# Optimization experiments

Hardware: AMD Instinct MI355X
Metric: run time of the kernel (lower is better)

Reference implementation:

```python
import jax, jax.numpy as jnp
import numpy as np

PAD_IDX = 0
PROTON_MASS = 1.007276
WATER_MASS = 18.010565
CO_MASS = 27.994915
MASS_TOL = 0.5
TEMPERATURE = 0.1
HUBER_DELTA = 0.2
CE_WEIGHT = 1.0
SPEC_WEIGHT = 0.1
T, B, S, V = 6, 512, 40, 28
N_PEAKS = 512


def setup_inputs() -> dict:
    key = jax.random.key(0)
    ks = jax.random.split(key, 7)
    all_logits = jax.random.normal(ks[0], (T, B, S, V), dtype=jnp.float32)
    targets = jax.random.randint(ks[1], (B, S), 0, V, dtype=jnp.int32)
    target_mask = jax.random.uniform(ks[2], (B, S)) > 0.2
    # observed peak m/z values in a realistic 100..2000 Da window, sorted per spectrum
    observed_masses = jnp.sort(
        100.0 + 1900.0 * jax.random.uniform(ks[3], (B, N_PEAKS), dtype=jnp.float32), axis=-1)
    observed_intensities = jax.random.uniform(ks[4], (B, N_PEAKS), dtype=jnp.float32)
    peak_mask = jax.random.uniform(ks[5], (B, N_PEAKS)) > 0.3
    # amino-acid residue masses; first 3 tokens are specials (PAD/SOS/EOS) -> mass 0
    aa = jnp.array([71.03711, 156.10111, 114.04293, 115.02694, 103.00919,
                    129.04259, 128.05858, 57.02146, 137.05891, 113.08406,
                    113.08406, 128.09496, 131.04049, 147.06841, 97.05276,
                    87.03203, 101.04768, 186.07931, 163.06333, 99.06841],
                   dtype=jnp.float32)
    aa_masses = jnp.concatenate([jnp.zeros(3, jnp.float32), aa,
                                 jnp.zeros(V - 3 - aa.shape[0], jnp.float32)])
    return {"all_logits": all_logits, "targets": targets, "target_mask": target_mask,
            "observed_masses": observed_masses, "observed_intensities": observed_intensities,
            "peak_mask": peak_mask, "aa_masses": aa_masses}


def _deep_supervision_loss(all_logits, targets, target_mask):
    # weights: linear 1..T, normalized
    w = jnp.arange(1, T + 1, dtype=jnp.float32)
    w = w / w.sum()
    logp = jax.nn.log_softmax(all_logits, axis=-1)            # [T,B,S,V]
    ce = -jnp.take_along_axis(logp, targets[None, :, :, None].astype(jnp.int32),
                              axis=-1)[..., 0]                # [T,B,S]
    ce = jnp.where(targets[None] == PAD_IDX, 0.0, ce)          # ignore_index
    mf = target_mask.astype(jnp.float32)                       # [B,S]
    denom = jnp.clip(mf.sum(), 1.0)
    per_step = (ce * mf[None]).sum(axis=(1, 2)) / denom        # [T]
    return (w * per_step).sum()


def _spectrum_loss(final_probs, observed_masses, observed_intensities, peak_mask, aa_masses):
    expected = jnp.einsum('bsv,v->bs', final_probs, aa_masses)   # [B,S]
    residue = expected[:, 1:-1]                                  # [B,S-2]
    b_ions = jnp.cumsum(residue, axis=1)[:, :-1] + PROTON_MASS   # [B,S-3]
    y_ions = jnp.flip(jnp.cumsum(jnp.flip(residue, 1), axis=1), 1)[:, :-1] + WATER_MASS + PROTON_MASS
    a_ions = b_ions - CO_MASS
    theo = jnp.concatenate([b_ions, y_ions, a_ions], axis=1)     # [B, 3*(S-3)]
    d = jnp.abs(theo[:, :, None] - observed_masses[:, None, :])  # [B,P,N]
    in_win = d < MASS_TOL
    mask = peak_mask[:, None, :] & in_win
    scores = jnp.where(mask, -d / TEMPERATURE, -jnp.inf)
    soft = jax.nn.softmax(scores, axis=-1)
    has = mask.any(axis=-1)                                      # [B,P]
    soft = jnp.where(has[..., None], soft, 0.0)                  # nan_to_num for all -inf rows
    dc = jnp.minimum(d, MASS_TOL)
    hub = jnp.where(dc <= HUBER_DELTA, 0.5 * dc * dc,
                    HUBER_DELTA * (dc - 0.5 * HUBER_DELTA))
    matched = (soft * hub).sum(axis=-1)                          # [B,P]
    iw = (soft * observed_intensities[:, None, :]).sum(axis=-1)  # [B,P]
    nm = has.astype(jnp.float32)
    return (matched * iw * nm).sum() / jnp.clip(nm.sum(), 1.0)


def reference(all_logits, targets, target_mask, observed_masses,
              observed_intensities, peak_mask, aa_masses):
    ce = _deep_supervision_loss(all_logits, targets, target_mask)
    final_probs = jax.nn.softmax(all_logits[-1], axis=-1)
    spec = _spectrum_loss(final_probs, observed_masses, observed_intensities,
                          peak_mask, aa_masses)
    return CE_WEIGHT * ce + SPEC_WEIGHT * spec
```

## Files before the change

### kernel.cpp

```cpp
#include <hip/hip_runtime.h>
#include <stdint.h>

#define TSTEPS 6
#define BB 512
#define SS 40
#define VV 28
#define NPK 512
#define NION 111
#define NROWS (TSTEPS * SS)
#define NBLK BB

#define PROTON 1.007276f
#define WATER 18.010565f
#define CO 27.994915f

__device__ __forceinline__ float4 blockReduceSum4(float4 v, float4* red4) {
#pragma unroll
  for (int off = 32; off > 0; off >>= 1) {
    v.x += __shfl_down(v.x, off); v.y += __shfl_down(v.y, off);
    v.z += __shfl_down(v.z, off); v.w += __shfl_down(v.w, off);
  }
  int lane = threadIdx.x & 63, wid = threadIdx.x >> 6;
  if (lane == 0) red4[wid] = v;
  __syncthreads();
  v = (threadIdx.x < 4) ? red4[threadIdx.x] : make_float4(0.f, 0.f, 0.f, 0.f);
  if (wid == 0) {
#pragma unroll
    for (int off = 2; off > 0; off >>= 1) {
      v.x += __shfl_down(v.x, off); v.y += __shfl_down(v.y, off);
      v.z += __shfl_down(v.z, off); v.w += __shfl_down(v.w, off);
    }
  }
  return v;
}

__global__ void __launch_bounds__(256) k_fused(
    const float* __restrict__ logits,
    const int* __restrict__ targets,
    const uint8_t* __restrict__ tmask8,
    const float* __restrict__ obs_m,
    const float* __restrict__ obs_i,
    const uint8_t* __restrict__ pmask8,
    const float* __restrict__ aa,
    float4* __restrict__ partial) {
  __shared__ __align__(16) float s_logit[NROWS * VV];
  __shared__ float s_mass[NPK];
  __shared__ float s_int[NPK];
  __shared__ float s_exp[SS];
  __shared__ float s_theo[NION + 1];
  __shared__ float s_aa[VV];
  __shared__ float4 red4[4];
  __shared__ int s_flt, s_flp;
  const int tid = threadIdx.x;
  const int b = blockIdx.x;
  float4 acc = make_float4(0.f, 0.f, 0.f, 0.f);

  {
    const float4* gl4 = (const float4*)logits;
    float4* l4 = (float4*)s_logit;
#pragma unroll
    for (int k = 0; k < 7; ++k) {
      int i = k * 256 + tid;
      if (i < 6 * 280) {
        int t = i / 280;
        int off = i - t * 280;
        l4[i] = gl4[(size_t)t * (BB * SS * VV / 4) + (size_t)b * 280 + off];
      }
    }
  }
  float m1 = obs_m[(size_t)b * NPK + tid];
  float m2 = obs_m[(size_t)b * NPK + 256 + tid];
  float i1 = obs_i[(size_t)b * NPK + tid];
  float i2 = obs_i[(size_t)b * NPK + 256 + tid];
  if (tid < VV) s_aa[tid] = aa[tid];
  if (tid < 64) {
    unsigned long long bl = __ballot(tmask8[4 * tid + 1] != 0);
    if (tid == 0) s_flt = (bl != 0ull) ? 1 : 0;
  } else if (tid < 128) {
    unsigned long long bl = __ballot(pmask8[4 * (tid - 64) + 1] != 0);
    if (tid == 64) s_flp = (bl != 0ull) ? 1 : 0;
  }
  __syncthreads();
  const int flt = s_flt, flp = s_flp;
  bool pm1 = flp ? (pmask8[(size_t)b * NPK + tid] != 0)
                 : (((const uint32_t*)pmask8)[(size_t)b * NPK + tid] != 0u);
  bool pm2 = flp ? (pmask8[(size_t)b * NPK + 256 + tid] != 0)
                 : (((const uint32_t*)pmask8)[(size_t)b * NPK + 256 + tid] != 0u);
  s_mass[tid] = m1;
  s_mass[256 + tid] = m2;
  s_int[tid] = pm1 ? i1 : -1.0f;
  s_int[256 + tid] = pm2 ? i2 : -1.0f;

  if (tid < NROWS) {
    const int t = tid / SS, spos = tid - t * SS;
    const float4* l4 = (const float4*)s_logit;
    float4 q0 = l4[tid * 7 + 0], q1 = l4[tid * 7 + 1], q2 = l4[tid * 7 + 2],
           q3 = l4[tid * 7 + 3], q4 = l4[tid * 7 + 4], q5 = l4[tid * 7 + 5],
           q6 = l4[tid * 7 + 6];
    float e0 = __expf(q0.x), e1 = __expf(q0.y), e2 = __expf(q0.z), e3 = __expf(q0.w);
    float e4 = __expf(q1.x), e5 = __expf(q1.y), e6 = __expf(q1.z), e7 = __expf(q1.w);
    float e8 = __expf(q2.x), e9 = __expf(q2.y), e10 = __expf(q2.z), e11 = __expf(q2.w);
    float e12 = __expf(q3.x), e13 = __expf(q3.y), e14 = __expf(q3.z), e15 = __expf(q3.w);
    float e16 = __expf(q4.x), e17 = __expf(q4.y), e18 = __expf(q4.z), e19 = __expf(q4.w);
    float e20 = __expf(q5.x), e21 = __expf(q5.y), e22 = __expf(q5.z), e23 = __expf(q5.w);
    float e24 = __expf(q6.x), e25 = __expf(q6.y), e26 = __expf(q6.z), e27 = __expf(q6.w);
    float se = (((e0 + e1) + (e2 + e3)) + ((e4 + e5) + (e6 + e7))) +
               (((e8 + e9) + (e10 + e11)) + ((e12 + e13) + (e14 + e15))) +
               (((e16 + e17) + (e18 + e19)) + ((e20 + e21) + (e22 + e23))) +
               ((e24 + e25) + (e26 + e27));
    float lse = __logf(se);
    const int bs = b * SS + spos;
    int tgt = targets[bs];
    bool msk = flt ? (tmask8[bs] != 0) : (((const uint32_t*)tmask8)[bs] != 0u);
    float mf = msk ? 1.0f : 0.0f;
    if (tgt != 0) {
      float w = (float)(t + 1) * (1.0f / 21.0f);
      acc.x = w * (lse - s_logit[tid * VV + tgt]) * mf;
    }
    if (t == 0) acc.y = mf;
    if (t == TSTEPS - 1) {
      float sw = e0 * s_aa[0] + e1 * s_aa[1] + e2 * s_aa[2] + e3 * s_aa[3] +
                 e4 * s_aa[4] + e5 * s_aa[5] + e6 * s_aa[6] + e7 * s_aa[7] +
                 e8 * s_aa[8] + e9 * s_aa[9] + e10 * s_aa[10] + e11 * s_aa[11] +
                 e12 * s_aa[12] + e13 * s_aa[13] + e14 * s_aa[14] + e15 * s_aa[15] +
                 e16 * s_aa[16] + e17 * s_aa[17] + e18 * s_aa[18] + e19 * s_aa[19] +
                 e20 * s_aa[20] + e21 * s_aa[21] + e22 * s_aa[22] + e23 * s_aa[23] +
                 e24 * s_aa[24] + e25 * s_aa[25] + e26 * s_aa[26] + e27 * s_aa[27];
      s_exp[spos] = sw / se;
    }
  }
  __syncthreads();

  if (tid == 0) {
    float c = 0.0f;
#pragma unroll
    for (int j = 0; j < 37; j++) {
      c += s_exp[1 + j];
      s_theo[j] = c + PROTON;
      s_theo[74 + j] = c + PROTON - CO;
    }
    float c2 = 0.0f;
#pragma unroll
    for (int j = 37; j >= 0; j--) {
      c2 += s_exp[1 + j];
      if (j <= 36) s_theo[37 + j] = c2 + WATER + PROTON;
    }
  }
  __syncthreads();

  if (tid < NION) {
    const float th = s_theo[tid];
    const float lim = th - 0.5f;
    int lo = 0, hi = NPK;
    while (lo < hi) {
      int mid = (lo + hi) >> 1;
      if (s_mass[mid] <= lim) lo = mid + 1; else hi = mid;
    }
    float sev = 0.0f, sh = 0.0f, si = 0.0f;
    int has = 0;
    for (int p = lo; p < NPK; ++p) {
      float ms = s_mass[p];
      if (!(ms < th + 0.5f)) break;
      float iv = s_int[p];
      if (iv < 0.0f) continue;
      float d = fabsf(th - ms);
      if (!(d < 0.5f)) continue;
      float e = __expf(-10.0f * d);
      float hub = (d <= 0.2f) ? (0.5f * d * d) : (0.2f * (d - 0.1f));
      sev += e; sh += e * hub; si += e * iv;
      has = 1;
    }
    if (has) {
      acc.z = (sh / sev) * (si / sev);
      acc.w = 1.0f;
    }
  }

  float4 r = blockReduceSum4(acc, red4);
  if (tid == 0) partial[blockIdx.x] = r;
}

__global__ void __launch_bounds__(256) k_final(const float4* __restrict__ partial,
                                               float* __restrict__ out) {
  __shared__ float4 red4[4];
  float4 a = make_float4(0.f, 0.f, 0.f, 0.f);
  for (int i = threadIdx.x; i < NBLK; i += 256) {
    float4 v = partial[i];
    a.x += v.x; a.y += v.y; a.z += v.z; a.w += v.w;
  }
  float4 r = blockReduceSum4(a, red4);
  if (threadIdx.x == 0) {
    float ce = r.x / fmaxf(r.y, 1.0f);
    float spec = r.z / fmaxf(r.w, 1.0f);
    out[0] = ce + 0.1f * spec;
  }
}

extern "C" void kernel_launch(void* const* d_in, const int* in_sizes, int n_in,
                              void* d_out, int out_size, void* d_ws, size_t ws_size,
                              hipStream_t stream) {
  const float* all_logits = (const float*)d_in[0];
  const int* targets = (const int*)d_in[1];
  const uint8_t* target_mask = (const uint8_t*)d_in[2];
  const float* obs_m = (const float*)d_in[3];
  const float* obs_i = (const float*)d_in[4];
  const uint8_t* peak_mask = (const uint8_t*)d_in[5];
  const float* aa = (const float*)d_in[6];
  float* out = (float*)d_out;

  float4* partial = (float4*)d_ws;

  k_fused<<<NBLK, 256, 0, stream>>>(all_logits, targets, target_mask,
                                    obs_m, obs_i, peak_mask, aa, partial);
  k_final<<<1, 256, 0, stream>>>(partial, out);
}
```

Measured before the change: 13.82 us.

## Use direct global-to-LDS loads, hoist mask loads, and compute ion prefix sums with wave scan

```diff
diff --git a/kernel.cpp b/kernel.cpp
--- a/kernel.cpp
+++ b/kernel.cpp
@@ -33,6 +33,17 @@
   }
   return v;
 }
+
+#if __has_builtin(__builtin_amdgcn_global_load_lds)
+#define USE_DMA 1
+__device__ __forceinline__ void gl_lds16(const float4* g, float4* l) {
+  __builtin_amdgcn_global_load_lds(
+      (const __attribute__((address_space(1))) float4*)g,
+      (__attribute__((address_space(3))) float4*)l, 16, 0, 0);
+}
+#else
+#define USE_DMA 0
+#endif
 
 __global__ void __launch_bounds__(256) k_fused(
     const float* __restrict__ logits,
@@ -46,33 +57,56 @@
   __shared__ __align__(16) float s_logit[NROWS * VV];
   __shared__ float s_mass[NPK];
   __shared__ float s_int[NPK];
-  __shared__ float s_exp[SS];
   __shared__ float s_theo[NION + 1];
   __shared__ float s_aa[VV];
   __shared__ float4 red4[4];
   __shared__ int s_flt, s_flp;
   const int tid = threadIdx.x;
   const int b = blockIdx.x;
+  const int lane = tid & 63, wid = tid >> 6;
   float4 acc = make_float4(0.f, 0.f, 0.f, 0.f);
 
-  {
-    const float4* gl4 = (const float4*)logits;
-    float4* l4 = (float4*)s_logit;
-#pragma unroll
-    for (int k = 0; k < 7; ++k) {
-      int i = k * 256 + tid;
-      if (i < 6 * 280) {
-        int t = i / 280;
-        int off = i - t * 280;
-        l4[i] = gl4[(size_t)t * (BB * SS * VV / 4) + (size_t)b * 280 + off];
-      }
-    }
-  }
+  const float4* gl4 = (const float4*)logits;
+  float4* l4 = (float4*)s_logit;
+#if USE_DMA
+#pragma unroll
+  for (int k = 0; k < 7; ++k) {
+    int i = k * 256 + tid;
+    if (i < 6 * 280) {
+      int t = i / 280, off = i - t * 280;
+      gl_lds16(gl4 + (size_t)t * (BB * SS * VV / 4) + (size_t)b * 280 + off,
+               l4 + k * 256 + wid * 64);
+    }
+  }
+#else
+#pragma unroll
+  for (int k = 0; k < 7; ++k) {
+    int i = k * 256 + tid;
+    if (i < 6 * 280) {
+      int t = i / 280, off = i - t * 280;
+      l4[i] = gl4[(size_t)t * (BB * SS * VV / 4) + (size_t)b * 280 + off];
+    }
+  }
+#endif
+
   float m1 = obs_m[(size_t)b * NPK + tid];
   float m2 = obs_m[(size_t)b * NPK + 256 + tid];
-  float i1 = obs_i[(size_t)b * NPK + tid];
-  float i2 = obs_i[(size_t)b * NPK + 256 + tid];
+  float i1v = obs_i[(size_t)b * NPK + tid];
+  float i2v = obs_i[(size_t)b * NPK + 256 + tid];
+  bool p81 = pmask8[(size_t)b * NPK + tid] != 0;
+  bool p82 = pmask8[(size_t)b * NPK + 256 + tid] != 0;
+  bool pw1 = ((const uint32_t*)pmask8)[(size_t)b * NPK + tid] != 0u;
+  bool pw2 = ((const uint32_t*)pmask8)[(size_t)b * NPK + 256 + tid] != 0u;
   if (tid < VV) s_aa[tid] = aa[tid];
+  int tgt = 0, t = 0, spos = 0;
+  bool m8 = false, mw = false;
+  if (tid < NROWS) {
+    t = tid / SS; spos = tid - t * SS;
+    const int bs = b * SS + spos;
+    tgt = targets[bs];
+    m8 = tmask8[bs] != 0;
+    mw = ((const uint32_t*)tmask8)[bs] != 0u;
+  }
   if (tid < 64) {
     unsigned long long bl = __ballot(tmask8[4 * tid + 1] != 0);
     if (tid == 0) s_flt = (bl != 0ull) ? 1 : 0;
@@ -81,19 +115,15 @@
     if (tid == 64) s_flp = (bl != 0ull) ? 1 : 0;
   }
   __syncthreads();
+
   const int flt = s_flt, flp = s_flp;
-  bool pm1 = flp ? (pmask8[(size_t)b * NPK + tid] != 0)
-                 : (((const uint32_t*)pmask8)[(size_t)b * NPK + tid] != 0u);
-  bool pm2 = flp ? (pmask8[(size_t)b * NPK + 256 + tid] != 0)
-                 : (((const uint32_t*)pmask8)[(size_t)b * NPK + 256 + tid] != 0u);
   s_mass[tid] = m1;
   s_mass[256 + tid] = m2;
-  s_int[tid] = pm1 ? i1 : -1.0f;
-  s_int[256 + tid] = pm2 ? i2 : -1.0f;
-
+  s_int[tid] = ((flp ? p81 : pw1) ? i1v : -1.0f);
+  s_int[256 + tid] = ((flp ? p82 : pw2) ? i2v : -1.0f);
+
+  float exp_mass = 0.0f;
   if (tid < NROWS) {
-    const int t = tid / SS, spos = tid - t * SS;
-    const float4* l4 = (const float4*)s_logit;
     float4 q0 = l4[tid * 7 + 0], q1 = l4[tid * 7 + 1], q2 = l4[tid * 7 + 2],
            q3 = l4[tid * 7 + 3], q4 = l4[tid * 7 + 4], q5 = l4[tid * 7 + 5],
            q6 = l4[tid * 7 + 6];
@@ -109,10 +139,7 @@
                (((e16 + e17) + (e18 + e19)) + ((e20 + e21) + (e22 + e23))) +
                ((e24 + e25) + (e26 + e27));
     float lse = __logf(se);
-    const int bs = b * SS + spos;
-    int tgt = targets[bs];
-    bool msk = flt ? (tmask8[bs] != 0) : (((const uint32_t*)tmask8)[bs] != 0u);
-    float mf = msk ? 1.0f : 0.0f;
+    float mf = (flt ? m8 : mw) ? 1.0f : 0.0f;
     if (tgt != 0) {
       float w = (float)(t + 1) * (1.0f / 21.0f);
       acc.x = w * (lse - s_logit[tid * VV + tgt]) * mf;
@@ -126,24 +153,25 @@
                  e16 * s_aa[16] + e17 * s_aa[17] + e18 * s_aa[18] + e19 * s_aa[19] +
                  e20 * s_aa[20] + e21 * s_aa[21] + e22 * s_aa[22] + e23 * s_aa[23] +
                  e24 * s_aa[24] + e25 * s_aa[25] + e26 * s_aa[26] + e27 * s_aa[27];
-      s_exp[spos] = sw / se;
-    }
-  }
-  __syncthreads();
-
-  if (tid == 0) {
-    float c = 0.0f;
-#pragma unroll
-    for (int j = 0; j < 37; j++) {
-      c += s_exp[1 + j];
-      s_theo[j] = c + PROTON;
-      s_theo[74 + j] = c + PROTON - CO;
-    }
-    float c2 = 0.0f;
-#pragma unroll
-    for (int j = 37; j >= 0; j--) {
-      c2 += s_exp[1 + j];
-      if (j <= 36) s_theo[37 + j] = c2 + WATER + PROTON;
+      exp_mass = sw / se;
+    }
+  }
+
+  if (wid == 3) {
+    float v = (t == TSTEPS - 1 && spos >= 1 && spos <= 38) ? exp_mass : 0.0f;
+    float p = v;
+#pragma unroll
+    for (int off = 1; off < 64; off <<= 1) {
+      float n = __shfl_up(p, off);
+      if (lane >= off) p += n;
+    }
+    float T = __shfl(p, 46);
+    float pprev = __shfl_up(p, 1);
+    if (lane >= 9 && lane <= 45) {
+      int j = lane - 9;
+      s_theo[j] = p + PROTON;
+      s_theo[74 + j] = p + PROTON - CO;
+      s_theo[37 + j] = T - pprev + WATER + PROTON;
     }
   }
   __syncthreads();
```

New measurement: 12.95 us. 1.07x faster.
